# Kernel tuning notes

Measured on AMD Instinct MI355X. Metric: run time of the kernel, lower is better.

Reference implementation:

```python
import jax, jax.numpy as jnp
import numpy as np

C = 256
CQK = C // 8  # 32

def setup_inputs() -> dict:
    key = jax.random.key(0)
    ks = jax.random.split(key, 9)
    B, H, W = 4, 64, 64
    s = 0.02
    return {
        "x": jax.random.normal(ks[0], (B, C, W, H), jnp.float32),
        "y": jax.random.normal(ks[1], (B, C, W, H), jnp.float32),
        "Wq": jax.random.normal(ks[2], (CQK, C), jnp.float32) * s,
        "bq": jax.random.normal(ks[3], (CQK,), jnp.float32) * s,
        "Wk": jax.random.normal(ks[4], (CQK, C), jnp.float32) * s,
        "bk": jax.random.normal(ks[5], (CQK,), jnp.float32) * s,
        "Wv": jax.random.normal(ks[6], (C, C), jnp.float32) * s,
        "bv": jax.random.normal(ks[7], (C,), jnp.float32) * s,
        "gamma": jnp.zeros((1,), jnp.float32) + 0.1,  # nonzero so output depends on attention
    }

def reference(x, y, Wq, bq, Wk, bk, Wv, bv, gamma):
    B, Cc, Wd, Hd = x.shape
    N = Wd * Hd
    xf = x.reshape(B, Cc, N)  # [B,C,N]
    yf = y.reshape(B, Cc, N)
    # 1x1 convs == channel matmuls
    q = jnp.einsum('dc,bcn->bnd', Wq, xf) + bq  # [B,N,CQK]
    k = jnp.einsum('dc,bcn->bdn', Wk, yf) + bk[None, :, None]  # [B,CQK,N]
    v = jnp.einsum('ec,bcn->ben', Wv, yf) + bv[None, :, None]  # [B,C,N]
    energy = jnp.einsum('bnd,bdm->bnm', q, k)  # [B,N,N]
    attn = jax.nn.softmax(energy, axis=-1)
    out = jnp.einsum('bem,bnm->ben', v, attn)  # [B,C,N]
    out = out.reshape(B, Cc, Wd, Hd)
    return gamma * out + x
```

## Files before the change

### kernel.cpp

```cpp
#include <hip/hip_runtime.h>
#include <hip/hip_bf16.h>
#include <stdint.h>

#define B_   4
#define C_   256
#define CQK_ 32
#define N_   4096

typedef float f32x4  __attribute__((ext_vector_type(4)));
typedef short bf16x8 __attribute__((ext_vector_type(8)));
typedef unsigned uint4v __attribute__((ext_vector_type(4)));

__device__ __forceinline__ unsigned short f2bf(float f) {
    unsigned u = __builtin_bit_cast(unsigned, f);
    u += 0x7FFFu + ((u >> 16) & 1u);
    return (unsigned short)(u >> 16);
}
__device__ __forceinline__ unsigned pack2(float a, float b) {
    return (unsigned)f2bf(a) | ((unsigned)f2bf(b) << 16);
}

__device__ __forceinline__ size_t vfrag_off(int b, int e, int m) {
    return ((((size_t)b * 128 + (m >> 5)) * 16 + (e >> 4)) * 64
            + (size_t)((m >> 3) & 3) * 16 + (e & 15)) * 8 + (m & 7);
}

__global__ __launch_bounds__(256) void transpose_kernel(
        const float* __restrict__ x, const float* __restrict__ y,
        const float* __restrict__ Wq, const float* __restrict__ Wk,
        const float* __restrict__ Wv,
        unsigned short* __restrict__ xb, unsigned short* __restrict__ yb,
        unsigned short* __restrict__ Wqb, unsigned short* __restrict__ Wkb,
        unsigned short* __restrict__ Wvb) {
    const int bid = blockIdx.x, tid = threadIdx.x;
    if (bid < 512) {
        __shared__ char lds[64 * 528];
        const bool isx = bid < 256;
        const int slab = bid & 255;
        const int b  = slab >> 6;
        const int n0 = (slab & 63) * 64;
        const float* __restrict__ src = isx ? x : y;
        unsigned short* __restrict__ dst = isx ? xb : yb;
        const int l = tid & 63, wv = tid >> 6;
        const float* sp = src + (size_t)(b * C_) * N_ + n0 + l;
#pragma unroll
        for (int i = 0; i < 64; i += 2) {
            const int c = wv * 64 + i;
            const float v0 = sp[(size_t)c * N_];
            const float v1 = sp[(size_t)(c + 1) * N_];
            *(unsigned*)(lds + l * 528 + c * 2) = pack2(v0, v1);
        }
        __syncthreads();
        const int n = tid >> 5, chunk = tid & 31;
#pragma unroll
        for (int j = 0; j < 8; ++j) {
            const int nn = n + j * 8;
            const uint4v v = *(const uint4v*)(lds + nn * 528 + chunk * 16);
            *(uint4v*)((char*)(dst + ((size_t)b * N_ + n0 + nn) * C_) + chunk * 16) = v;
        }
    } else {
        for (int p = (bid - 512) * 256 + tid; p < 40960; p += 64 * 256) {
            const float* s; unsigned short* d; int off;
            if (p < 4096)      { s = Wq; d = Wqb; off = p; }
            else if (p < 8192) { s = Wk; d = Wkb; off = p - 4096; }
            else               { s = Wv; d = Wvb; off = p - 8192; }
            *(unsigned*)(d + off * 2) = pack2(s[off * 2], s[off * 2 + 1]);
        }
    }
}

__global__ __launch_bounds__(256) void proj_gemm(
        const unsigned short* __restrict__ xb, const unsigned short* __restrict__ yb,
        const unsigned short* __restrict__ Wqb, const unsigned short* __restrict__ Wkb,
        const unsigned short* __restrict__ Wvb,
        const float* __restrict__ bq, const float* __restrict__ bk,
        const float* __restrict__ bv,
        unsigned short* __restrict__ qf, unsigned short* __restrict__ kf,
        unsigned short* __restrict__ vf) {
    const int tid = threadIdx.x, w = tid >> 6, l = tid & 63;
    const int lr = l & 15, lg = l >> 4;
    const int gid = blockIdx.x;
    const int b  = (gid >> 1) & 3;
    const int n0 = ((((gid >> 3) << 1) | (gid & 1))) * 64;

    f32x4 accV[4][4];
    f32x4 accQ[4];
#pragma unroll
    for (int e = 0; e < 4; ++e)
#pragma unroll
        for (int m = 0; m < 4; ++m) accV[e][m] = (f32x4){0.f, 0.f, 0.f, 0.f};
#pragma unroll
    for (int m = 0; m < 4; ++m) accQ[m] = (f32x4){0.f, 0.f, 0.f, 0.f};

    const unsigned short* __restrict__ Wqk = (w < 2) ? Wqb : Wkb;
    const int d0 = (w & 1) * 16;

#pragma unroll
    for (int ks = 0; ks < 8; ++ks) {
        const int c0 = ks * 32 + lg * 8;
        bf16x8 aY[4], aS[4];
#pragma unroll
        for (int mb = 0; mb < 4; ++mb)
            aY[mb] = *(const bf16x8*)(yb + ((size_t)b * N_ + n0 + mb * 16 + lr) * C_ + c0);
        if (w < 2) {
#pragma unroll
            for (int mb = 0; mb < 4; ++mb)
                aS[mb] = *(const bf16x8*)(xb + ((size_t)b * N_ + n0 + mb * 16 + lr) * C_ + c0);
        } else {
#pragma unroll
            for (int mb = 0; mb < 4; ++mb) aS[mb] = aY[mb];
        }
        bf16x8 bV[4];
#pragma unroll
        for (int eb = 0; eb < 4; ++eb)
            bV[eb] = *(const bf16x8*)(Wvb + (size_t)(w * 64 + eb * 16 + lr) * C_ + c0);
        const bf16x8 bQ = *(const bf16x8*)(Wqk + (size_t)(d0 + lr) * C_ + c0);
#pragma unroll
        for (int eb = 0; eb < 4; ++eb)
#pragma unroll
            for (int mb = 0; mb < 4; ++mb)
                accV[eb][mb] = __builtin_amdgcn_mfma_f32_16x16x32_bf16(
                    aY[mb], bV[eb], accV[eb][mb], 0, 0, 0);
#pragma unroll
        for (int mb = 0; mb < 4; ++mb)
            accQ[mb] = __builtin_amdgcn_mfma_f32_16x16x32_bf16(aS[mb], bQ, accQ[mb], 0, 0, 0);
    }

#pragma unroll
    for (int eb = 0; eb < 4; ++eb) {
        const int e = w * 64 + eb * 16 + lr;
        const float bve = bv[e];
#pragma unroll
        for (int mb = 0; mb < 4; ++mb) {
            const size_t off = vfrag_off(b, e, n0 + mb * 16 + lg * 4);
            unsigned* p = (unsigned*)(vf + off);
            p[0] = pack2(accV[eb][mb][0] + bve, accV[eb][mb][1] + bve);
            p[1] = pack2(accV[eb][mb][2] + bve, accV[eb][mb][3] + bve);
        }
    }
    const float bqv = ((w < 2) ? bq : bk)[d0 + lr];
    unsigned short* __restrict__ dqk = (w < 2) ? qf : kf;
#pragma unroll
    for (int mb = 0; mb < 4; ++mb)
#pragma unroll
        for (int r = 0; r < 4; ++r) {
            const int n = n0 + mb * 16 + lg * 4 + r;
            dqk[((size_t)b * N_ + n) * CQK_ + d0 + lr] = f2bf(accQ[mb][r] + bqv);
        }
}

__global__ __launch_bounds__(512, 2) void attn_kernel(
        const unsigned short* __restrict__ qf, const unsigned short* __restrict__ kf,
        const unsigned short* __restrict__ vf, const float* __restrict__ x,
        const float* __restrict__ gamma, float* __restrict__ out) {
    __shared__ char plds[2][64 * 272];
    __shared__ float oslab[2][64][128];
    __shared__ float cLs[8][64];
    __shared__ float cLt[64];
    const int tid = threadIdx.x, w = tid >> 6, l = tid & 63;
    const int lr = l & 15, lg = l >> 4;
    const int gid = blockIdx.x;
    const int b  = (gid >> 1) & 3;
    const int q0 = ((((gid >> 3) << 1) | (gid & 1))) * 64;
    const int eh = w >> 2, ksw = w & 3;

    bf16x8 qfr[4];
#pragma unroll
    for (int qblk = 0; qblk < 4; ++qblk)
        qfr[qblk] = *(const bf16x8*)(
            qf + ((size_t)b * N_ + q0 + qblk * 16 + lr) * CQK_ + lg * 8);

    f32x4 acc[4][8];
#pragma unroll
    for (int i = 0; i < 4; ++i)
#pragma unroll
        for (int j = 0; j < 8; ++j) acc[i][j] = (f32x4){0.f, 0.f, 0.f, 0.f};
    float Lacc[4] = {0.f, 0.f, 0.f, 0.f};

    const unsigned short* kbase = kf + ((size_t)b * N_ + w * 16 + lr) * CQK_ + lg * 8;

#define PREF_K(T, K)                                                           \
    K = *(const bf16x8*)(kbase + (size_t)(((T) & 31) * 128) * CQK_);

#define PREF_V(T)                                                              \
    {                                                                          \
        const int t_ = (T) & 31;                                               \
        _Pragma("unroll")                                                      \
        for (int ebi_ = 0; ebi_ < 8; ++ebi_)                                   \
            vV[ebi_] = *(const bf16x8*)(                                       \
                vf + ((size_t)((b * 128 + t_ * 4 + ksw) * 16 + eh * 8 + ebi_)) \
                         * 512 + l * 8);                                       \
    }

#define BODY(T, K)                                                             \
    {                                                                          \
        f32x4 e4_[4];                                                          \
        _Pragma("unroll")                                                      \
        for (int qblk = 0; qblk < 4; ++qblk)                                   \
            e4_[qblk] = __builtin_amdgcn_mfma_f32_16x16x32_bf16(               \
                K, qfr[qblk], (f32x4){0.f, 0.f, 0.f, 0.f}, 0, 0, 0);           \
        char* pw_ = plds[(T) & 1];                                             \
        const int m2_ = w * 16 + lg * 4;                                       \
        _Pragma("unroll")                                                      \
        for (int qblk = 0; qblk < 4; ++qblk) {                                 \
            const float p0 = __expf(e4_[qblk][0]);                             \
            const float p1 = __expf(e4_[qblk][1]);                             \
            const float p2 = __expf(e4_[qblk][2]);                             \
            const float p3 = __expf(e4_[qblk][3]);                             \
            Lacc[qblk] += (p0 + p1) + (p2 + p3);                               \
            unsigned u0, u1;                                                   \
            asm("v_cvt_pk_bf16_f32 %0, %1, %2" : "=v"(u0) : "v"(p0), "v"(p1)); \
            asm("v_cvt_pk_bf16_f32 %0, %1, %2" : "=v"(u1) : "v"(p2), "v"(p3)); \
            const int q_ = qblk * 16 + lr;                                     \
            const int byte_ = q_ * 272 + ((m2_ >> 3) << 4) + (m2_ & 7) * 2;    \
            *(unsigned long long*)(pw_ + byte_) =                              \
                (unsigned long long)u0 | ((unsigned long long)u1 << 32);       \
        }                                                                      \
        asm volatile("s_waitcnt lgkmcnt(0)" ::: "memory");                     \
        __builtin_amdgcn_s_barrier();                                          \
        asm volatile("" ::: "memory");                                         \
        PREF_K((T) + 2, K);                                                    \
        __builtin_amdgcn_s_setprio(1);                                         \
        _Pragma("unroll")                                                      \
        for (int qblk = 0; qblk < 4; ++qblk) {                                 \
            const int q_ = qblk * 16 + lr;                                     \
            const bf16x8 pa_ = *(const bf16x8*)(                               \
                pw_ + q_ * 272 + ((ksw * 4 + lg) << 4));                       \
            _Pragma("unroll")                                                  \
            for (int ebi_ = 0; ebi_ < 8; ++ebi_)                               \
                acc[qblk][ebi_] = __builtin_amdgcn_mfma_f32_16x16x32_bf16(     \
                    pa_, vV[ebi_], acc[qblk][ebi_], 0, 0, 0);                  \
        }                                                                      \
        __builtin_amdgcn_s_setprio(0);                                         \
        PREF_V((T) + 1);                  \
    }

    bf16x8 kA, kB, vV[8];
    PREF_K(0, kA);
    PREF_K(1, kB);
    PREF_V(0);

    for (int kt = 0; kt < 32; kt += 2) {
        BODY(kt, kA);
        BODY(kt + 1, kB);
    }
#undef PREF_K
#undef PREF_V
#undef BODY

#pragma unroll
    for (int qblk = 0; qblk < 4; ++qblk) {
        Lacc[qblk] += __shfl_xor(Lacc[qblk], 16);
        Lacc[qblk] += __shfl_xor(Lacc[qblk], 32);
    }
    if (l < 16) {
#pragma unroll
        for (int qblk = 0; qblk < 4; ++qblk) cLs[w][qblk * 16 + lr] = Lacc[qblk];
    }
    __syncthreads();
    if (tid < 64) {
        float s = 0.f;
#pragma unroll
        for (int w2 = 0; w2 < 8; ++w2) s += cLs[w2][tid];
        cLt[tid] = 1.0f / s;
    }
    __syncthreads();

#pragma unroll
    for (int round = 3; round > 0; --round) {
        if (ksw == round) {
#pragma unroll
            for (int qblk = 0; qblk < 4; ++qblk)
#pragma unroll
                for (int ebi = 0; ebi < 8; ++ebi)
#pragma unroll
                    for (int r = 0; r < 4; ++r)
                        oslab[eh][qblk * 16 + lg * 4 + r][ebi * 16 + lr] = acc[qblk][ebi][r];
        }
        __syncthreads();
        if (ksw == round - 1) {
#pragma unroll
            for (int qblk = 0; qblk < 4; ++qblk)
#pragma unroll
                for (int ebi = 0; ebi < 8; ++ebi)
#pragma unroll
                    for (int r = 0; r < 4; ++r)
                        acc[qblk][ebi][r] += oslab[eh][qblk * 16 + lg * 4 + r][ebi * 16 + lr];
        }
        __syncthreads();
    }
    if (ksw == 0) {
#pragma unroll
        for (int qblk = 0; qblk < 4; ++qblk)
#pragma unroll
            for (int ebi = 0; ebi < 8; ++ebi)
#pragma unroll
                for (int r = 0; r < 4; ++r)
                    oslab[eh][qblk * 16 + lg * 4 + r][ebi * 16 + lr] = acc[qblk][ebi][r];
    }
    __syncthreads();

    const float g = gamma[0];
#pragma unroll
    for (int qblk = 0; qblk < 4; ++qblk) {
        float rI[4];
#pragma unroll
        for (int r = 0; r < 4; ++r) rI[r] = cLt[qblk * 16 + lg * 4 + r];
        const int nb = q0 + qblk * 16 + lg * 4;
#pragma unroll
        for (int ebi = 0; ebi < 2; ++ebi) {
            const int e = (w * 2 + ebi) * 16 + lr;
            const size_t idx = ((size_t)b * C_ + e) * N_ + nb;
            const f32x4 xv = *(const f32x4*)(x + idx);
            f32x4 ov;
#pragma unroll
            for (int r = 0; r < 4; ++r) {
                const float val = oslab[e >> 7][qblk * 16 + lg * 4 + r][e & 127];
                ov[r] = g * val * rI[r] + xv[r];
            }
            *(f32x4*)(out + idx) = ov;
        }
    }
}

extern "C" void kernel_launch(void* const* d_in, const int* in_sizes, int n_in,
                              void* d_out, int out_size, void* d_ws, size_t ws_size,
                              hipStream_t stream) {
    (void)in_sizes; (void)n_in; (void)out_size; (void)ws_size;
    const float* x     = (const float*)d_in[0];
    const float* y     = (const float*)d_in[1];
    const float* Wq    = (const float*)d_in[2];
    const float* bq    = (const float*)d_in[3];
    const float* Wk    = (const float*)d_in[4];
    const float* bk    = (const float*)d_in[5];
    const float* Wv    = (const float*)d_in[6];
    const float* bv    = (const float*)d_in[7];
    const float* gamma = (const float*)d_in[8];
    float* out = (float*)d_out;

    unsigned short* qf  = (unsigned short*)d_ws;
    unsigned short* kf  = qf + (size_t)B_ * N_ * CQK_;
    unsigned short* vf  = kf + (size_t)B_ * N_ * CQK_;
    unsigned short* Wqb = vf + (size_t)B_ * N_ * C_;
    unsigned short* Wkb = Wqb + CQK_ * C_;
    unsigned short* Wvb = Wkb + CQK_ * C_;

    unsigned short* xb = (unsigned short*)d_out;
    unsigned short* yb = xb + (size_t)B_ * N_ * C_;

    transpose_kernel<<<dim3(576), 256, 0, stream>>>(x, y, Wq, Wk, Wv, xb, yb, Wqb, Wkb, Wvb);
    proj_gemm<<<dim3(256), 256, 0, stream>>>(xb, yb, Wqb, Wkb, Wvb, bq, bk, bv, qf, kf, vf);
    attn_kernel<<<dim3(256), 512, 0, stream>>>(qf, kf, vf, x, gamma, out);
}
```

Baseline: 75.82 us.

## Fuse x/y transpose into projection GEMM and restructure attention loop pipelining

```diff
diff --git a/kernel.cpp b/kernel.cpp
--- a/kernel.cpp
+++ b/kernel.cpp
@@ -25,64 +25,60 @@
             + (size_t)((m >> 3) & 3) * 16 + (e & 15)) * 8 + (m & 7);
 }
 
-__global__ __launch_bounds__(256) void transpose_kernel(
-        const float* __restrict__ x, const float* __restrict__ y,
+__global__ __launch_bounds__(256) void wconv_kernel(
         const float* __restrict__ Wq, const float* __restrict__ Wk,
         const float* __restrict__ Wv,
-        unsigned short* __restrict__ xb, unsigned short* __restrict__ yb,
         unsigned short* __restrict__ Wqb, unsigned short* __restrict__ Wkb,
         unsigned short* __restrict__ Wvb) {
-    const int bid = blockIdx.x, tid = threadIdx.x;
-    if (bid < 512) {
-        __shared__ char lds[64 * 528];
-        const bool isx = bid < 256;
-        const int slab = bid & 255;
-        const int b  = slab >> 6;
-        const int n0 = (slab & 63) * 64;
-        const float* __restrict__ src = isx ? x : y;
-        unsigned short* __restrict__ dst = isx ? xb : yb;
-        const int l = tid & 63, wv = tid >> 6;
-        const float* sp = src + (size_t)(b * C_) * N_ + n0 + l;
-#pragma unroll
-        for (int i = 0; i < 64; i += 2) {
-            const int c = wv * 64 + i;
-            const float v0 = sp[(size_t)c * N_];
-            const float v1 = sp[(size_t)(c + 1) * N_];
-            *(unsigned*)(lds + l * 528 + c * 2) = pack2(v0, v1);
-        }
-        __syncthreads();
-        const int n = tid >> 5, chunk = tid & 31;
-#pragma unroll
-        for (int j = 0; j < 8; ++j) {
-            const int nn = n + j * 8;
-            const uint4v v = *(const uint4v*)(lds + nn * 528 + chunk * 16);
-            *(uint4v*)((char*)(dst + ((size_t)b * N_ + n0 + nn) * C_) + chunk * 16) = v;
-        }
-    } else {
-        for (int p = (bid - 512) * 256 + tid; p < 40960; p += 64 * 256) {
-            const float* s; unsigned short* d; int off;
-            if (p < 4096)      { s = Wq; d = Wqb; off = p; }
-            else if (p < 8192) { s = Wk; d = Wkb; off = p - 4096; }
-            else               { s = Wv; d = Wvb; off = p - 8192; }
-            *(unsigned*)(d + off * 2) = pack2(s[off * 2], s[off * 2 + 1]);
-        }
+    for (int p = blockIdx.x * 256 + threadIdx.x; p < 40960; p += 64 * 256) {
+        const float* s; unsigned short* d; int off;
+        if (p < 4096)      { s = Wq; d = Wqb; off = p; }
+        else if (p < 8192) { s = Wk; d = Wkb; off = p - 4096; }
+        else               { s = Wv; d = Wvb; off = p - 8192; }
+        *(unsigned*)(d + off * 2) = pack2(s[off * 2], s[off * 2 + 1]);
     }
 }
 
 __global__ __launch_bounds__(256) void proj_gemm(
-        const unsigned short* __restrict__ xb, const unsigned short* __restrict__ yb,
+        const float* __restrict__ x, const float* __restrict__ y,
         const unsigned short* __restrict__ Wqb, const unsigned short* __restrict__ Wkb,
         const unsigned short* __restrict__ Wvb,
         const float* __restrict__ bq, const float* __restrict__ bk,
         const float* __restrict__ bv,
         unsigned short* __restrict__ qf, unsigned short* __restrict__ kf,
         unsigned short* __restrict__ vf) {
+    __shared__ char xlds[64 * 512];
+    __shared__ char ylds[64 * 512];
     const int tid = threadIdx.x, w = tid >> 6, l = tid & 63;
     const int lr = l & 15, lg = l >> 4;
     const int gid = blockIdx.x;
     const int b  = (gid >> 1) & 3;
     const int n0 = ((((gid >> 3) << 1) | (gid & 1))) * 64;
 
+    {
+        const int j = l & 7;
+        const float* spx = x + (size_t)b * C_ * N_ + n0 + l;
+        const float* spy = y + (size_t)b * C_ * N_ + n0 + l;
+#pragma unroll
+        for (int gl = 0; gl < 8; ++gl) {
+            const int c8 = w * 64 + gl * 8;
+            const int slot = (gl + j) & 7;
+            uint4v px, py;
+#pragma unroll
+            for (int t = 0; t < 4; ++t) {
+                px[t] = pack2(spx[(size_t)(c8 + 2 * t) * N_], spx[(size_t)(c8 + 2 * t + 1) * N_]);
+                py[t] = pack2(spy[(size_t)(c8 + 2 * t) * N_], spy[(size_t)(c8 + 2 * t + 1) * N_]);
+            }
+            *(uint4v*)(xlds + l * 512 + w * 128 + slot * 16) = px;
+            *(uint4v*)(ylds + l * 512 + w * 128 + slot * 16) = py;
+        }
+    }
+    __syncthreads();
+
+#define AFRAG(LDS, ROW, G)                                                     \
+    (*(const bf16x8*)((LDS) + (ROW) * 512 + ((G) >> 3) * 128                   \
+                      + ((((G) & 7) + ((ROW) & 7)) & 7) * 16))
+
     f32x4 accV[4][4];
     f32x4 accQ[4];
 #pragma unroll
@@ -98,14 +94,13 @@
 #pragma unroll
     for (int ks = 0; ks < 8; ++ks) {
         const int c0 = ks * 32 + lg * 8;
+        const int g  = ks * 4 + lg;
         bf16x8 aY[4], aS[4];
 #pragma unroll
-        for (int mb = 0; mb < 4; ++mb)
-            aY[mb] = *(const bf16x8*)(yb + ((size_t)b * N_ + n0 + mb * 16 + lr) * C_ + c0);
+        for (int mb = 0; mb < 4; ++mb) aY[mb] = AFRAG(ylds, mb * 16 + lr, g);
         if (w < 2) {
 #pragma unroll
-            for (int mb = 0; mb < 4; ++mb)
-                aS[mb] = *(const bf16x8*)(xb + ((size_t)b * N_ + n0 + mb * 16 + lr) * C_ + c0);
+            for (int mb = 0; mb < 4; ++mb) aS[mb] = AFRAG(xlds, mb * 16 + lr, g);
         } else {
 #pragma unroll
             for (int mb = 0; mb < 4; ++mb) aS[mb] = aY[mb];
@@ -125,6 +120,7 @@
         for (int mb = 0; mb < 4; ++mb)
             accQ[mb] = __builtin_amdgcn_mfma_f32_16x16x32_bf16(aS[mb], bQ, accQ[mb], 0, 0, 0);
     }
+#undef AFRAG
 
 #pragma unroll
     for (int eb = 0; eb < 4; ++eb) {
@@ -153,10 +149,11 @@
         const unsigned short* __restrict__ qf, const unsigned short* __restrict__ kf,
         const unsigned short* __restrict__ vf, const float* __restrict__ x,
         const float* __restrict__ gamma, float* __restrict__ out) {
-    __shared__ char plds[2][64 * 272];
-    __shared__ float oslab[2][64][128];
-    __shared__ float cLs[8][64];
-    __shared__ float cLt[64];
+    __shared__ char arena[4 * 17408 + 8 * 64 * 4 + 64 * 4];
+    char* plds = arena;
+    float* cLs = (float*)(arena + 4 * 17408);
+    float* cLt = cLs + 8 * 64;
+    auto oslab = (float (*)[64][128])arena;
     const int tid = threadIdx.x, w = tid >> 6, l = tid & 63;
     const int lr = l & 15, lg = l >> 4;
     const int gid = blockIdx.x;
@@ -174,32 +171,31 @@
 #pragma unroll
     for (int i = 0; i < 4; ++i)
 #pragma unroll
-        for (int j = 0; j < 8; ++j) acc[i][j] = (f32x4){0.f, 0.f, 0.f, 0.f};
+        for (int jj = 0; jj < 8; ++jj) acc[i][jj] = (f32x4){0.f, 0.f, 0.f, 0.f};
     float Lacc[4] = {0.f, 0.f, 0.f, 0.f};
 
     const unsigned short* kbase = kf + ((size_t)b * N_ + w * 16 + lr) * CQK_ + lg * 8;
 
+#define PBUF(T) (plds + ((T) & 3) * 17408)
 #define PREF_K(T, K)                                                           \
     K = *(const bf16x8*)(kbase + (size_t)(((T) & 31) * 128) * CQK_);
-
-#define PREF_V(T)                                                              \
+#define PREF_V(T, VV)                                                          \
     {                                                                          \
         const int t_ = (T) & 31;                                               \
         _Pragma("unroll")                                                      \
         for (int ebi_ = 0; ebi_ < 8; ++ebi_)                                   \
-            vV[ebi_] = *(const bf16x8*)(                                       \
+            VV[ebi_] = *(const bf16x8*)(                                       \
                 vf + ((size_t)((b * 128 + t_ * 4 + ksw) * 16 + eh * 8 + ebi_)) \
                          * 512 + l * 8);                                       \
     }
-
-#define BODY(T, K)                                                             \
+#define QKEXP(T, K)                                                            \
     {                                                                          \
         f32x4 e4_[4];                                                          \
         _Pragma("unroll")                                                      \
         for (int qblk = 0; qblk < 4; ++qblk)                                   \
             e4_[qblk] = __builtin_amdgcn_mfma_f32_16x16x32_bf16(               \
                 K, qfr[qblk], (f32x4){0.f, 0.f, 0.f, 0.f}, 0, 0, 0);           \
-        char* pw_ = plds[(T) & 1];                                             \
+        char* pw_ = PBUF(T);                                                   \
         const int m2_ = w * 16 + lg * 4;                                       \
         _Pragma("unroll")                                                      \
         for (int qblk = 0; qblk < 4; ++qblk) {                                 \
@@ -216,11 +212,10 @@
             *(unsigned long long*)(pw_ + byte_) =                              \
                 (unsigned long long)u0 | ((unsigned long long)u1 << 32);       \
         }                                                                      \
-        asm volatile("s_waitcnt lgkmcnt(0)" ::: "memory");                     \
-        __builtin_amdgcn_s_barrier();                                          \
-        asm volatile("" ::: "memory");                                         \
-        PREF_K((T) + 2, K);                                                    \
-        __builtin_amdgcn_s_setprio(1);                                         \
+    }
+#define PVQ(T, VV)                                                             \
+    {                                                                          \
+        char* pw_ = PBUF(T);                                                   \
         _Pragma("unroll")                                                      \
         for (int qblk = 0; qblk < 4; ++qblk) {                                 \
             const int q_ = qblk * 16 + lr;                                     \
@@ -229,24 +224,38 @@
             _Pragma("unroll")                                                  \
             for (int ebi_ = 0; ebi_ < 8; ++ebi_)                               \
                 acc[qblk][ebi_] = __builtin_amdgcn_mfma_f32_16x16x32_bf16(     \
-                    pa_, vV[ebi_], acc[qblk][ebi_], 0, 0, 0);                  \
+                    pa_, VV[ebi_], acc[qblk][ebi_], 0, 0, 0);                  \
         }                                                                      \
-        __builtin_amdgcn_s_setprio(0);                                         \
-        PREF_V((T) + 1);                  \
-    }
-
-    bf16x8 kA, kB, vV[8];
+    }
+
+    bf16x8 kA, kB, vVA[8], vVB[8];
     PREF_K(0, kA);
     PREF_K(1, kB);
-    PREF_V(0);
+    PREF_V(0, vVA);
+    PREF_V(1, vVB);
 
     for (int kt = 0; kt < 32; kt += 2) {
-        BODY(kt, kA);
-        BODY(kt + 1, kB);
-    }
+        QKEXP(kt, kA);
+        QKEXP(kt + 1, kB);
+        asm volatile("s_waitcnt lgkmcnt(0)" ::: "memory");
+        __builtin_amdgcn_s_barrier();
+        asm volatile("" ::: "memory");
+        PREF_K(kt + 2, kA);
+        PREF_K(kt + 3, kB);
+        __builtin_amdgcn_s_setprio(1);
+        PVQ(kt, vVA);
+        __builtin_amdgcn_s_setprio(0);
+        PREF_V(kt + 2, vVA);
+        __builtin_amdgcn_s_setprio(1);
+        PVQ(kt + 1, vVB);
+        __builtin_amdgcn_s_setprio(0);
+        PREF_V(kt + 3, vVB);
+    }
+#undef PBUF
 #undef PREF_K
 #undef PREF_V
-#undef BODY
+#undef QKEXP
+#undef PVQ
 
 #pragma unroll
     for (int qblk = 0; qblk < 4; ++qblk) {
@@ -255,13 +264,13 @@
     }
     if (l < 16) {
 #pragma unroll
-        for (int qblk = 0; qblk < 4; ++qblk) cLs[w][qblk * 16 + lr] = Lacc[qblk];
+        for (int qblk = 0; qblk < 4; ++qblk) cLs[w * 64 + qblk * 16 + lr] = Lacc[qblk];
     }
     __syncthreads();
     if (tid < 64) {
         float s = 0.f;
 #pragma unroll
-        for (int w2 = 0; w2 < 8; ++w2) s += cLs[w2][tid];
+        for (int w2 = 0; w2 < 8; ++w2) s += cLs[w2 * 64 + tid];
         cLt[tid] = 1.0f / s;
     }
     __syncthreads();
@@ -345,10 +354,7 @@
     unsigned short* Wkb = Wqb + CQK_ * C_;
     unsigned short* Wvb = Wkb + CQK_ * C_;
 
-    unsigned short* xb = (unsigned short*)d_out;
-    unsigned short* yb = xb + (size_t)B_ * N_ * C_;
-
-    transpose_kernel<<<dim3(576), 256, 0, stream>>>(x, y, Wq, Wk, Wv, xb, yb, Wqb, Wkb, Wvb);
-    proj_gemm<<<dim3(256), 256, 0, stream>>>(xb, yb, Wqb, Wkb, Wvb, bq, bk, bv, qf, kf, vf);
+    wconv_kernel<<<dim3(64), 256, 0, stream>>>(Wq, Wk, Wv, Wqb, Wkb, Wvb);
+    proj_gemm<<<dim3(256), 256, 0, stream>>>(x, y, Wqb, Wkb, Wvb, bq, bk, bv, qf, kf, vf);
     attn_kernel<<<dim3(256), 512, 0, stream>>>(qf, kf, vf, x, gamma, out);
 }
```

New measurement: 121.3 us. 60.0% more time.

## Fuse x/y transpose and bf16 conversion into projection GEMM via swizzled LDS

Applied to the files above, without the earlier changes.

```diff
diff --git a/kernel.cpp b/kernel.cpp
--- a/kernel.cpp
+++ b/kernel.cpp
@@ -25,64 +25,60 @@
             + (size_t)((m >> 3) & 3) * 16 + (e & 15)) * 8 + (m & 7);
 }
 
-__global__ __launch_bounds__(256) void transpose_kernel(
-        const float* __restrict__ x, const float* __restrict__ y,
+__global__ __launch_bounds__(256) void wconv_kernel(
         const float* __restrict__ Wq, const float* __restrict__ Wk,
         const float* __restrict__ Wv,
-        unsigned short* __restrict__ xb, unsigned short* __restrict__ yb,
         unsigned short* __restrict__ Wqb, unsigned short* __restrict__ Wkb,
         unsigned short* __restrict__ Wvb) {
-    const int bid = blockIdx.x, tid = threadIdx.x;
-    if (bid < 512) {
-        __shared__ char lds[64 * 528];
-        const bool isx = bid < 256;
-        const int slab = bid & 255;
-        const int b  = slab >> 6;
-        const int n0 = (slab & 63) * 64;
-        const float* __restrict__ src = isx ? x : y;
-        unsigned short* __restrict__ dst = isx ? xb : yb;
-        const int l = tid & 63, wv = tid >> 6;
-        const float* sp = src + (size_t)(b * C_) * N_ + n0 + l;
-#pragma unroll
-        for (int i = 0; i < 64; i += 2) {
-            const int c = wv * 64 + i;
-            const float v0 = sp[(size_t)c * N_];
-            const float v1 = sp[(size_t)(c + 1) * N_];
-            *(unsigned*)(lds + l * 528 + c * 2) = pack2(v0, v1);
-        }
-        __syncthreads();
-        const int n = tid >> 5, chunk = tid & 31;
-#pragma unroll
-        for (int j = 0; j < 8; ++j) {
-            const int nn = n + j * 8;
-            const uint4v v = *(const uint4v*)(lds + nn * 528 + chunk * 16);
-            *(uint4v*)((char*)(dst + ((size_t)b * N_ + n0 + nn) * C_) + chunk * 16) = v;
-        }
-    } else {
-        for (int p = (bid - 512) * 256 + tid; p < 40960; p += 64 * 256) {
-            const float* s; unsigned short* d; int off;
-            if (p < 4096)      { s = Wq; d = Wqb; off = p; }
-            else if (p < 8192) { s = Wk; d = Wkb; off = p - 4096; }
-            else               { s = Wv; d = Wvb; off = p - 8192; }
-            *(unsigned*)(d + off * 2) = pack2(s[off * 2], s[off * 2 + 1]);
-        }
+    for (int p = blockIdx.x * 256 + threadIdx.x; p < 40960; p += 64 * 256) {
+        const float* s; unsigned short* d; int off;
+        if (p < 4096)      { s = Wq; d = Wqb; off = p; }
+        else if (p < 8192) { s = Wk; d = Wkb; off = p - 4096; }
+        else               { s = Wv; d = Wvb; off = p - 8192; }
+        *(unsigned*)(d + off * 2) = pack2(s[off * 2], s[off * 2 + 1]);
     }
 }
 
 __global__ __launch_bounds__(256) void proj_gemm(
-        const unsigned short* __restrict__ xb, const unsigned short* __restrict__ yb,
+        const float* __restrict__ x, const float* __restrict__ y,
         const unsigned short* __restrict__ Wqb, const unsigned short* __restrict__ Wkb,
         const unsigned short* __restrict__ Wvb,
         const float* __restrict__ bq, const float* __restrict__ bk,
         const float* __restrict__ bv,
         unsigned short* __restrict__ qf, unsigned short* __restrict__ kf,
         unsigned short* __restrict__ vf) {
+    __shared__ char xlds[64 * 512];
+    __shared__ char ylds[64 * 512];
     const int tid = threadIdx.x, w = tid >> 6, l = tid & 63;
     const int lr = l & 15, lg = l >> 4;
     const int gid = blockIdx.x;
     const int b  = (gid >> 1) & 3;
     const int n0 = ((((gid >> 3) << 1) | (gid & 1))) * 64;
 
+    {
+        const int j = l & 7;
+        const float* spx = x + (size_t)b * C_ * N_ + n0 + l;
+        const float* spy = y + (size_t)b * C_ * N_ + n0 + l;
+#pragma unroll
+        for (int gl = 0; gl < 8; ++gl) {
+            const int c8 = w * 64 + gl * 8;
+            const int slot = (gl + j) & 7;
+            uint4v px, py;
+#pragma unroll
+            for (int t = 0; t < 4; ++t) {
+                px[t] = pack2(spx[(size_t)(c8 + 2 * t) * N_], spx[(size_t)(c8 + 2 * t + 1) * N_]);
+                py[t] = pack2(spy[(size_t)(c8 + 2 * t) * N_], spy[(size_t)(c8 + 2 * t + 1) * N_]);
+            }
+            *(uint4v*)(xlds + l * 512 + w * 128 + slot * 16) = px;
+            *(uint4v*)(ylds + l * 512 + w * 128 + slot * 16) = py;
+        }
+    }
+    __syncthreads();
+
+#define AFRAG(LDS, ROW, G)                                                     \
+    (*(const bf16x8*)((LDS) + (ROW) * 512 + ((G) >> 3) * 128                   \
+                      + ((((G) & 7) + ((ROW) & 7)) & 7) * 16))
+
     f32x4 accV[4][4];
     f32x4 accQ[4];
 #pragma unroll
@@ -98,14 +94,13 @@
 #pragma unroll
     for (int ks = 0; ks < 8; ++ks) {
         const int c0 = ks * 32 + lg * 8;
+        const int g  = ks * 4 + lg;
         bf16x8 aY[4], aS[4];
 #pragma unroll
-        for (int mb = 0; mb < 4; ++mb)
-            aY[mb] = *(const bf16x8*)(yb + ((size_t)b * N_ + n0 + mb * 16 + lr) * C_ + c0);
+        for (int mb = 0; mb < 4; ++mb) aY[mb] = AFRAG(ylds, mb * 16 + lr, g);
         if (w < 2) {
 #pragma unroll
-            for (int mb = 0; mb < 4; ++mb)
-                aS[mb] = *(const bf16x8*)(xb + ((size_t)b * N_ + n0 + mb * 16 + lr) * C_ + c0);
+            for (int mb = 0; mb < 4; ++mb) aS[mb] = AFRAG(xlds, mb * 16 + lr, g);
         } else {
 #pragma unroll
             for (int mb = 0; mb < 4; ++mb) aS[mb] = aY[mb];
@@ -125,6 +120,7 @@
         for (int mb = 0; mb < 4; ++mb)
             accQ[mb] = __builtin_amdgcn_mfma_f32_16x16x32_bf16(aS[mb], bQ, accQ[mb], 0, 0, 0);
     }
+#undef AFRAG
 
 #pragma unroll
     for (int eb = 0; eb < 4; ++eb) {
@@ -345,10 +341,7 @@
     unsigned short* Wkb = Wqb + CQK_ * C_;
     unsigned short* Wvb = Wkb + CQK_ * C_;
 
-    unsigned short* xb = (unsigned short*)d_out;
-    unsigned short* yb = xb + (size_t)B_ * N_ * C_;
-
-    transpose_kernel<<<dim3(576), 256, 0, stream>>>(x, y, Wq, Wk, Wv, xb, yb, Wqb, Wkb, Wvb);
-    proj_gemm<<<dim3(256), 256, 0, stream>>>(xb, yb, Wqb, Wkb, Wvb, bq, bk, bv, qf, kf, vf);
+    wconv_kernel<<<dim3(64), 256, 0, stream>>>(Wq, Wk, Wv, Wqb, Wkb, Wvb);
+    proj_gemm<<<dim3(256), 256, 0, stream>>>(x, y, Wqb, Wkb, Wvb, bq, bk, bv, qf, kf, vf);
     attn_kernel<<<dim3(256), 512, 0, stream>>>(qf, kf, vf, x, gamma, out);
 }
```

After: 70.04 us (median of 2 runs). 7.6% less time.
